# Kernel optimization log

Hardware: AMD Instinct MI355X
Metric: run time of the kernel (lower is better)

The kernel has to match this reference:

```python
import jax, jax.numpy as jnp
import numpy as np

N = 128          # system size (8*8*2), hard-coded in SpectrumLoss
M_LANCZOS = 10   # Lanczos(m=10)
KAPPA = 0.276


def dd_opt(x, U1, kappa):
    # Wilson-style 2D hopping operator (stand-in for the external DDOpt).
    # x: (B,8,8,2) fields, U1: (B,8,8,2) real gauge links (2 directions).
    u0 = U1[..., 0:1]
    u1 = U1[..., 1:2]
    hop = (u0 * jnp.roll(x, -1, axis=1)
           + u1 * jnp.roll(x, -1, axis=2)
           + jnp.roll(u0 * x, 1, axis=1)
           + jnp.roll(u1 * x, 1, axis=2))
    return x - kappa * hop


def build_lower_tri(net_out):
    # Row-major packing of a lower-triangular NxN matrix (torch.tril_indices order).
    B = net_out.shape[0]
    r, c = jnp.tril_indices(N)
    L = jnp.zeros((B, N, N), net_out.dtype)
    return L.at[:, r, c].set(net_out)


def matvect(L, U1, x):
    # x: (B, N). Preconditioned operator: L (L^T (D x)).
    B = x.shape[0]
    y = dd_opt(x.reshape(B, 8, 8, 2), U1, KAPPA).reshape(B, N)
    y = jnp.einsum('bij,bi->bj', L, y)  # upper_tri_mat: M^H v (real -> M^T v)
    y = jnp.einsum('bij,bj->bi', L, y)  # lower_tri_matvect: L v
    return y


def lanczos(Av, v0):
    # Standard batched Lanczos producing symmetric tridiagonal T (B, M, M).
    B = v0.shape[0]

    def step(carry, _):
        v_prev, v_cur, beta = carry
        w = Av(v_cur)
        alpha = jnp.sum(w * v_cur, axis=1)
        w = w - alpha[:, None] * v_cur - beta[:, None] * v_prev
        beta_new = jnp.linalg.norm(w, axis=1)
        v_next = w / (beta_new[:, None] + 1e-30)
        return (v_cur, v_next, beta_new), (alpha, beta_new)

    init = (jnp.zeros_like(v0), v0, jnp.zeros((B,), v0.dtype))
    _, (alphas, betas) = jax.lax.scan(step, init, None, length=M_LANCZOS)
    alphas = alphas.T  # (B, M)
    betas = betas.T    # (B, M); last beta unused
    T = jnp.zeros((B, M_LANCZOS, M_LANCZOS), v0.dtype)
    i = jnp.arange(M_LANCZOS)
    T = T.at[:, i, i].set(alphas)
    j = jnp.arange(M_LANCZOS - 1)
    T = T.at[:, j, j + 1].set(betas[:, :-1])
    T = T.at[:, j + 1, j].set(betas[:, :-1])
    return T


def setup_inputs() -> dict:
    key = jax.random.key(0)
    k1, k2, k3 = jax.random.split(key, 3)
    B = 2048
    net_out = jax.random.normal(k1, (B, N * (N + 1) // 2), dtype=jnp.float32)
    U1 = jax.random.uniform(k2, (B, 8, 8, 2), dtype=jnp.float32)
    v = jax.random.normal(k3, (B, N), dtype=jnp.float32)
    return {"net_out": net_out, "U1": U1, "v": v}


def reference(net_out, U1, v):
    vn = v / jnp.linalg.norm(v, axis=1, keepdims=True)
    L = build_lower_tri(net_out)
    T = lanczos(lambda x: matvect(L, U1, x), vn)
    eig = jnp.abs(jnp.linalg.eigvalsh(T))  # symmetric tridiagonal -> real eigvals
    max_e = jnp.max(eig, axis=1)
    min_e = jnp.min(eig, axis=1)
    return jnp.mean(max_e ** 2) - jnp.mean(min_e ** 2)
```

## Files before the change

kernel.cpp:

```cpp
#include <hip/hip_runtime.h>
#include <hip/hip_bf16.h>
#include <math.h>

#define NN 128
#define TRI 8256
#define BATCH 2048
#define M_L 10
#define KAPPA 0.276f
#define LDL 136

using half8 = __attribute__((ext_vector_type(8))) _Float16;
using half2v = __attribute__((ext_vector_type(2))) _Float16;
using f32x4  = __attribute__((ext_vector_type(4))) float;

static __device__ inline float dot2h(unsigned m, unsigned y, float c) {
#if __has_builtin(__builtin_amdgcn_fdot2)
    return __builtin_amdgcn_fdot2(__builtin_bit_cast(half2v, m),
                                  __builtin_bit_cast(half2v, y), c, false);
#else
    half2v a = __builtin_bit_cast(half2v, m), b = __builtin_bit_cast(half2v, y);
    return c + (float)a.x * (float)b.x + (float)a.y * (float)b.y;
#endif
}

__global__ __launch_bounds__(256, 4) void lanczos_kernel(
    const float* __restrict__ net_out,
    const float* __restrict__ U1,
    const float* __restrict__ v_in,
    float* __restrict__ ab_out)
{
    __shared__ __align__(16) _Float16 Lsq[128 * LDL];
    __shared__ float u0s[64], u1s[64];
    __shared__ __align__(16) float xv[NN];
    __shared__ __align__(16) _Float16 yh[NN];
    __shared__ __align__(16) float part[256];
    __shared__ float red[4];

    const int b = blockIdx.x;
    const int t = threadIdx.x;
    const int lane = t & 63;
    const int w = t >> 6;

    {
        unsigned long long* z = (unsigned long long*)Lsq;
        #pragma unroll
        for (int k = t; k < 128 * LDL * 2 / 8; k += 256) z[k] = 0ULL;
    }
    if (t < 64) {
        const float2* uu = (const float2*)(U1 + (size_t)b * 128);
        float2 p = uu[t];
        u0s[t] = p.x; u1s[t] = p.y;
    }
    float vt = 0.0f;
    if (t < 128) vt = v_in[(size_t)b * NN + t];
    __syncthreads();

    {
        const int r = t & 127, q = t >> 7;
        const int len = r + 1;
        const int lo = (q * len) >> 1, hi = ((q + 1) * len) >> 1;
        const float* src = net_out + (size_t)b * TRI + (r * (r + 1)) / 2;
        _Float16* dst = &Lsq[r * LDL];
        for (int c = lo; c < hi; c++) dst[c] = (_Float16)src[c];
    }
    {
        float s = vt * vt;
        #pragma unroll
        for (int o = 32; o > 0; o >>= 1) s += __shfl_down(s, o, 64);
        if (lane == 0 && t < 128) red[w] = s;
    }
    __syncthreads();

    float ib = 1.0f / sqrtf(red[0] + red[1]);
    if (t < 128) xv[t] = vt;

    {
        const int m = lane & 15;
        const int g = lane >> 4;
        f32x4 acc[2][8];
        #pragma unroll
        for (int bi = 0; bi < 2; bi++)
            #pragma unroll
            for (int j = 0; j < 8; j++) acc[bi][j] = (f32x4){0.f, 0.f, 0.f, 0.f};
        const int band0 = w, band1 = w + 4;
        #pragma unroll
        for (int kc = 0; kc < 4; kc++) {
            const int col = kc * 32 + g * 8;
            half8 a0 = *(const half8*)&Lsq[(16 * band0 + m) * LDL + col];
            half8 a1 = *(const half8*)&Lsq[(16 * band1 + m) * LDL + col];
            #pragma unroll
            for (int j = 0; j < 8; j++) {
                half8 bfr = *(const half8*)&Lsq[(16 * j + m) * LDL + col];
                acc[0][j] = __builtin_amdgcn_mfma_f32_16x16x32_f16(a0, bfr, acc[0][j], 0, 0, 0);
                acc[1][j] = __builtin_amdgcn_mfma_f32_16x16x32_f16(a1, bfr, acc[1][j], 0, 0, 0);
            }
        }
        __syncthreads();

        #pragma unroll
        for (int bi = 0; bi < 2; bi++) {
            const int band = (bi == 0) ? band0 : band1;
            #pragma unroll
            for (int j = 0; j < 8; j++) {
                f32x4 a = acc[bi][j];
                half2v p01 = {(_Float16)a[0], (_Float16)a[1]};
                half2v p23 = {(_Float16)a[2], (_Float16)a[3]};
                uint2 pk;
                pk.x = __builtin_bit_cast(unsigned, p01);
                pk.y = __builtin_bit_cast(unsigned, p23);
                *(uint2*)&Lsq[(16 * j + m) * LDL + 16 * band + 4 * g] = pk;
            }
        }
    }

    const int si = t >> 4, sj = (t >> 1) & 7, ss = t & 1;
    const int ip = (si + 1) & 7, im = (si + 7) & 7;
    const int jp = (sj + 1) & 7, jm = (sj + 7) & 7;
    const int idx_ip = (ip << 4) | (sj << 1) | ss;
    const int idx_jp = (si << 4) | (jp << 1) | ss;
    const int idx_im = (im << 4) | (sj << 1) | ss;
    const int idx_jm = (si << 4) | (jm << 1) | ss;

    float pvf = 0.0f, beta = 0.0f;
    __syncthreads();

    for (int m_it = 0; m_it < M_L; m_it++) {
        if (t < 128) {
            float x_t = xv[t];
            float hop = u0s[si * 8 + sj] * xv[idx_ip]
                      + u1s[si * 8 + sj] * xv[idx_jp]
                      + u0s[im * 8 + sj] * xv[idx_im]
                      + u1s[si * 8 + jm] * xv[idx_jm];
            yh[t] = (_Float16)(ib * (x_t - KAPPA * hop));
        }
        __syncthreads();

        {
            const int r = t & 127, h = t >> 7;
            const uint4* M4 = (const uint4*)&Lsq[r * LDL + 64 * h];
            const uint4* Y4 = (const uint4*)&yh[64 * h];
            float acc = 0.f;
            #pragma unroll
            for (int c = 0; c < 8; c++) {
                uint4 mv = M4[c];
                uint4 yv4 = Y4[c];
                acc = dot2h(mv.x, yv4.x, acc);
                acc = dot2h(mv.y, yv4.y, acc);
                acc = dot2h(mv.z, yv4.z, acc);
                acc = dot2h(mv.w, yv4.w, acc);
            }
            part[t] = acc;
        }
        __syncthreads();

        float wacc = 0.f, xcur = 0.f;
        if (t < 128) {
            wacc = part[t] + part[t + 128];
            xcur = xv[t] * ib;
            float s = wacc * xcur;
            #pragma unroll
            for (int o = 32; o > 0; o >>= 1) s += __shfl_down(s, o, 64);
            if (lane == 0) red[w] = s;
        }
        __syncthreads();

        if (t < 128) {
            float alpha = red[0] + red[1];
            wacc -= alpha * xcur + beta * pvf;
            xv[t] = wacc;
            float s = wacc * wacc;
            #pragma unroll
            for (int o = 32; o > 0; o >>= 1) s += __shfl_down(s, o, 64);
            if (lane == 0) red[2 + w] = s;
            if (t == 0) ab_out[(size_t)b * 20 + m_it] = red[0] + red[1];
        }
        __syncthreads();

        float beta_new = sqrtf(red[2] + red[3]);
        if (t == 0) ab_out[(size_t)b * 20 + 10 + m_it] = beta_new;
        if (t < 128) pvf = xcur;
        beta = beta_new;
        ib = 1.0f / (beta_new + 1e-30f);
    }
}

__device__ inline int sturm_count10(const double* a, const double* off2, double x) {
    double pm = 1.0;
    double p  = a[0] - x;
    int c = (p < 0.0);
    #pragma unroll
    for (int i = 1; i < M_L; i++) {
        double pn = (a[i] - x) * p - off2[i - 1] * pm;
        c += ((pn < 0.0) != (p < 0.0));
        if (fabs(pn) > 1e150) { pn *= 1e-150; p *= 1e-150; }
        pm = p; p = pn;
    }
    return c;
}

__device__ inline double msect_smallest(const double* a, const double* off2,
                                        double lo, double hi, int K, int lane) {
    for (int round = 0; round < 4; round++) {
        double wdt = (hi - lo) * (1.0 / 65.0);
        double x = lo + wdt * (double)(lane + 1);
        int cnt = sturm_count10(a, off2, x);
        unsigned long long mask = __ballot(cnt >= K);
        if (mask == 0ULL) {
            lo = lo + wdt * 64.0;
        } else {
            int p = __ffsll(mask) - 1;
            hi = lo + wdt * (double)(p + 1);
            if (p > 0) lo = lo + wdt * (double)p;
        }
    }
    return 0.5 * (lo + hi);
}

__device__ inline double msect_window(const double* a, const double* off2,
                                      double maxabs, int lane) {
    double lo = 0.0, hi = maxabs;
    for (int round = 0; round < 4; round++) {
        double wdt = (hi - lo) * (1.0 / 65.0);
        double s = lo + wdt * (double)(lane + 1);
        int inwin = sturm_count10(a, off2, s) - sturm_count10(a, off2, -s);
        unsigned long long mask = __ballot(inwin >= 1);
        if (mask == 0ULL) {
            lo = lo + wdt * 64.0;
        } else {
            int p = __ffsll(mask) - 1;
            hi = lo + wdt * (double)(p + 1);
            if (p > 0) lo = lo + wdt * (double)p;
        }
    }
    return 0.5 * (lo + hi);
}

__global__ __launch_bounds__(256) void eig_kernel(
    const float* __restrict__ ab, float* __restrict__ contrib)
{
    const int lane = threadIdx.x & 63;
    const int b = blockIdx.x * 4 + (threadIdx.x >> 6);
    if (b >= BATCH) return;
    const float* p = ab + (size_t)b * 20;
    double a[M_L], off2[M_L - 1], offa[M_L - 1];
    #pragma unroll
    for (int i = 0; i < M_L; i++) a[i] = (double)p[i];
    #pragma unroll
    for (int i = 0; i < M_L - 1; i++) {
        double bb = (double)p[10 + i];
        offa[i] = fabs(bb);
        off2[i] = bb * bb;
    }
    double lo = 1e300, hi = -1e300;
    #pragma unroll
    for (int i = 0; i < M_L; i++) {
        double r = 0.0;
        if (i > 0) r += offa[i - 1];
        if (i < M_L - 1) r += offa[i];
        lo = fmin(lo, a[i] - r);
        hi = fmax(hi, a[i] + r);
    }
    double lmax = msect_smallest(a, off2, lo, hi, M_L, lane);
    double lmin = msect_smallest(a, off2, lo, hi, 1,   lane);
    double maxabs = fmax(fabs(lmax), fabs(lmin));
    double minabs = msect_window(a, off2, maxabs, lane);
    if (lane == 0) contrib[b] = (float)(maxabs * maxabs - minabs * minabs);
}

__global__ __launch_bounds__(1024) void reduce_kernel(
    const float* __restrict__ contrib, float* __restrict__ out)
{
    __shared__ float red[16];
    int t = threadIdx.x;
    float s = contrib[t] + contrib[t + 1024];
    #pragma unroll
    for (int o = 32; o > 0; o >>= 1) s += __shfl_down(s, o, 64);
    if ((t & 63) == 0) red[t >> 6] = s;
    __syncthreads();
    if (t < 64) {
        float r = (t < 16) ? red[t] : 0.0f;
        #pragma unroll
        for (int o = 8; o > 0; o >>= 1) r += __shfl_down(r, o, 64);
        if (t == 0) out[0] = r / (float)BATCH;
    }
}

extern "C" void kernel_launch(void* const* d_in, const int* in_sizes, int n_in,
                              void* d_out, int out_size, void* d_ws, size_t ws_size,
                              hipStream_t stream) {
    const float* net_out = (const float*)d_in[0];
    const float* U1      = (const float*)d_in[1];
    const float* v       = (const float*)d_in[2];
    float* ab      = (float*)d_ws;
    float* contrib = ab + (size_t)BATCH * 20;

    lanczos_kernel<<<BATCH, 256, 0, stream>>>(net_out, U1, v, ab);
    eig_kernel<<<BATCH / 4, 256, 0, stream>>>(ab, contrib);
    reduce_kernel<<<1, 1024, 0, stream>>>(contrib, (float*)d_out);
}
```

Measured before the change: 147.4 us.

## Fuse Lanczos reductions into one pass and vectorize triangular load

```diff
diff --git a/kernel.cpp b/kernel.cpp
--- a/kernel.cpp
+++ b/kernel.cpp
@@ -9,7 +9,7 @@
 #define KAPPA 0.276f
 #define LDL 136
 
-using half8 = __attribute__((ext_vector_type(8))) _Float16;
+using half8  = __attribute__((ext_vector_type(8))) _Float16;
 using half2v = __attribute__((ext_vector_type(2))) _Float16;
 using f32x4  = __attribute__((ext_vector_type(4))) float;
 
@@ -33,8 +33,7 @@
     __shared__ float u0s[64], u1s[64];
     __shared__ __align__(16) float xv[NN];
     __shared__ __align__(16) _Float16 yh[NN];
-    __shared__ __align__(16) float part[256];
-    __shared__ float red[4];
+    __shared__ float red[6];
 
     const int b = blockIdx.x;
     const int t = threadIdx.x;
@@ -56,12 +55,22 @@
     __syncthreads();
 
     {
-        const int r = t & 127, q = t >> 7;
-        const int len = r + 1;
-        const int lo = (q * len) >> 1, hi = ((q + 1) * len) >> 1;
-        const float* src = net_out + (size_t)b * TRI + (r * (r + 1)) / 2;
-        _Float16* dst = &Lsq[r * LDL];
-        for (int c = lo; c < hi; c++) dst[c] = (_Float16)src[c];
+        const float4* src4 = (const float4*)(net_out + (size_t)b * TRI);
+        for (int q = t; q < TRI / 4; q += 256) {
+            float4 f = src4[q];
+            int e = 4 * q;
+            int r = (int)((sqrtf(8.0f * (float)e + 1.0f) - 1.0f) * 0.5f);
+            while ((r + 1) * (r + 2) / 2 <= e) r++;
+            while (r * (r + 1) / 2 > e) r--;
+            int c = e - r * (r + 1) / 2;
+            Lsq[r * LDL + c] = (_Float16)f.x;
+            c++; if (c > r) { r++; c = 0; }
+            Lsq[r * LDL + c] = (_Float16)f.y;
+            c++; if (c > r) { r++; c = 0; }
+            Lsq[r * LDL + c] = (_Float16)f.z;
+            c++; if (c > r) { r++; c = 0; }
+            Lsq[r * LDL + c] = (_Float16)f.w;
+        }
     }
     {
         float s = vt * vt;
@@ -71,8 +80,12 @@
     }
     __syncthreads();
 
-    float ib = 1.0f / sqrtf(red[0] + red[1]);
-    if (t < 128) xv[t] = vt;
+    float xcur = 0.0f;
+    if (t < 128) {
+        float nrm = sqrtf(red[0] + red[1]);
+        xcur = vt / nrm;
+        xv[t] = xcur;
+    }
 
     {
         const int m = lane & 15;
@@ -126,22 +139,21 @@
 
     for (int m_it = 0; m_it < M_L; m_it++) {
         if (t < 128) {
-            float x_t = xv[t];
             float hop = u0s[si * 8 + sj] * xv[idx_ip]
                       + u1s[si * 8 + sj] * xv[idx_jp]
                       + u0s[im * 8 + sj] * xv[idx_im]
                       + u1s[si * 8 + jm] * xv[idx_jm];
-            yh[t] = (_Float16)(ib * (x_t - KAPPA * hop));
+            yh[t] = (_Float16)(xcur - KAPPA * hop);
         }
         __syncthreads();
 
-        {
-            const int r = t & 127, h = t >> 7;
-            const uint4* M4 = (const uint4*)&Lsq[r * LDL + 64 * h];
-            const uint4* Y4 = (const uint4*)&yh[64 * h];
+        float z = 0.0f;
+        if (t < 128) {
+            const uint4* M4 = (const uint4*)&Lsq[t * LDL];
+            const uint4* Y4 = (const uint4*)yh;
             float acc = 0.f;
             #pragma unroll
-            for (int c = 0; c < 8; c++) {
+            for (int c = 0; c < 16; c++) {
                 uint4 mv = M4[c];
                 uint4 yv4 = Y4[c];
                 acc = dot2h(mv.x, yv4.x, acc);
@@ -149,38 +161,38 @@
                 acc = dot2h(mv.z, yv4.z, acc);
                 acc = dot2h(mv.w, yv4.w, acc);
             }
-            part[t] = acc;
-        }
-        __syncthreads();
-
-        float wacc = 0.f, xcur = 0.f;
-        if (t < 128) {
-            wacc = part[t] + part[t + 128];
-            xcur = xv[t] * ib;
-            float s = wacc * xcur;
-            #pragma unroll
-            for (int o = 32; o > 0; o >>= 1) s += __shfl_down(s, o, 64);
-            if (lane == 0) red[w] = s;
+            z = acc;
+            float s1 = z * xcur;
+            float s2 = z * z;
+            float s3 = z * pvf;
+            #pragma unroll
+            for (int o = 32; o > 0; o >>= 1) {
+                s1 += __shfl_down(s1, o, 64);
+                s2 += __shfl_down(s2, o, 64);
+                s3 += __shfl_down(s3, o, 64);
+            }
+            if (lane == 0) { red[w] = s1; red[2 + w] = s2; red[4 + w] = s3; }
         }
         __syncthreads();
 
         if (t < 128) {
             float alpha = red[0] + red[1];
-            wacc -= alpha * xcur + beta * pvf;
-            xv[t] = wacc;
-            float s = wacc * wacc;
-            #pragma unroll
-            for (int o = 32; o > 0; o >>= 1) s += __shfl_down(s, o, 64);
-            if (lane == 0) red[2 + w] = s;
-            if (t == 0) ab_out[(size_t)b * 20 + m_it] = red[0] + red[1];
+            float z2    = red[2] + red[3];
+            float zp    = red[4] + red[5];
+            float b2 = z2 - alpha * alpha - beta * (2.0f * zp - beta);
+            float beta_new = sqrtf(fmaxf(b2, 0.0f));
+            float wv = z - alpha * xcur - beta * pvf;
+            float xn = wv / (beta_new + 1e-30f);
+            pvf = xcur;
+            xcur = xn;
+            xv[t] = xn;
+            beta = beta_new;
+            if (t == 0) {
+                ab_out[(size_t)b * 20 + m_it]      = alpha;
+                ab_out[(size_t)b * 20 + 10 + m_it] = beta_new;
+            }
         }
         __syncthreads();
-
-        float beta_new = sqrtf(red[2] + red[3]);
-        if (t == 0) ab_out[(size_t)b * 20 + 10 + m_it] = beta_new;
-        if (t < 128) pvf = xcur;
-        beta = beta_new;
-        ib = 1.0f / (beta_new + 1e-30f);
     }
 }
 
```

Measured after the change: 140.1 us. -5.0%, faster.
